# Performance work log

Hardware: AMD Instinct MI355X
Metric: run time of the kernel (lower is better)

The kernel has to match this reference:

```python
import jax, jax.numpy as jnp
import numpy as np


def setup_inputs() -> dict:
    key = jax.random.key(0)
    k1, k2, k3, k4 = jax.random.split(key, 4)
    B, T, C, H = 8, 2048, 768, 64
    x = jax.random.normal(k1, (B, T, C), dtype=jnp.float32)
    # nn.Linear(n_embd, head_size, bias=False): weight [H, C]; stored here as [C, H] for x @ W
    Wk = jax.random.normal(k2, (C, H), dtype=jnp.float32) * (C ** -0.5)
    Wq = jax.random.normal(k3, (C, H), dtype=jnp.float32) * (C ** -0.5)
    Wv = jax.random.normal(k4, (C, H), dtype=jnp.float32) * (C ** -0.5)
    return {"x": x, "Wk": Wk, "Wq": Wq, "Wv": Wv}


def reference(x, Wk, Wq, Wv):
    # x: [B, T, C]
    C = x.shape[-1]
    k = jnp.einsum("btc,ch->bth", x, Wk)  # [B, T, H]
    q = jnp.einsum("btc,ch->bth", x, Wq)  # [B, T, H]
    v = jnp.einsum("btc,ch->bth", x, Wv)  # [B, T, H]
    # NOTE: source scales by C**-0.5 where C = n_embd (input channels), not head_size
    wei = jnp.einsum("bth,bsh->bts", q, k) * (C ** -0.5)  # [B, T, T]
    wei = jax.nn.softmax(wei, axis=-1)
    # dropout p=0.0 (eval): identity
    out = jnp.einsum("bts,bsh->bth", wei, v)  # [B, T, H]
    return out
```

## Files before the change

### kernel.cpp

```cpp
#include <hip/hip_runtime.h>


typedef __attribute__((ext_vector_type(4))) float f32x4;
typedef __attribute__((ext_vector_type(8))) unsigned short u16x8;
typedef __attribute__((ext_vector_type(8))) __bf16 bf16x8;
typedef __attribute__((ext_vector_type(8))) _Float16 f16x8;

#define LDR 72
#define LDT 40
#define KSCALE (0.03608439182435161f * 1.4426950408889634f)
#define PBIAS 4.0f

__device__ __forceinline__ unsigned short f2bf(float f) {
  unsigned int u = __float_as_uint(f);
  u += 0x7FFFu + ((u >> 16) & 1u);
  return (unsigned short)(u >> 16);
}
__device__ __forceinline__ unsigned short hi16(float f) {
  return (unsigned short)(__float_as_uint(f) >> 16);
}
__device__ __forceinline__ f32x4 mfma_bf16(u16x8 a, u16x8 b, f32x4 c) {
  return __builtin_amdgcn_mfma_f32_16x16x32_bf16(
      __builtin_bit_cast(bf16x8, a), __builtin_bit_cast(bf16x8, b), c, 0, 0, 0);
}
__device__ __forceinline__ void cp32B(unsigned short* dst, const unsigned short* src) {
  *(u16x8*)dst = *(const u16x8*)src;
  *(u16x8*)(dst + 8) = *(const u16x8*)(src + 8);
}

__global__ __launch_bounds__(256) void wconv_k(const float* __restrict__ Wk,
                                               const float* __restrict__ Wq,
                                               const float* __restrict__ Wv,
                                               unsigned short* __restrict__ wt) {
  __shared__ unsigned short tr[64 * LDR];
  const int w = blockIdx.x / 12;
  const int kt = blockIdx.x - w * 12;
  const float* W = (w == 0) ? Wk : ((w == 1) ? Wq : Wv);
  const int tid = threadIdx.x;
  const int kr = tid >> 2;
  const int n0 = (tid & 3) * 16;
  const f32x4* src = (const f32x4*)(W + (size_t)(kt * 64 + kr) * 64 + n0);
  f32x4 a0 = src[0], a1 = src[1], a2 = src[2], a3 = src[3];
#pragma unroll
  for (int j = 0; j < 4; ++j) {
    tr[(n0 + j) * LDR + kr] = f2bf(a0[j]);
    tr[(n0 + 4 + j) * LDR + kr] = f2bf(a1[j]);
    tr[(n0 + 8 + j) * LDR + kr] = f2bf(a2[j]);
    tr[(n0 + 12 + j) * LDR + kr] = f2bf(a3[j]);
  }
  __syncthreads();
  const int n = tid >> 2, kc = (tid & 3) * 16;
  cp32B(&wt[(size_t)(w * 64 + n) * 768 + kt * 64 + kc], &tr[n * LDR + kc]);
}

__global__ __launch_bounds__(256) void proj_k(const float* __restrict__ x,
                                              const unsigned short* __restrict__ wt,
                                              unsigned short* __restrict__ kg,
                                              unsigned short* __restrict__ qg,
                                              unsigned short* __restrict__ vt) {
  __shared__ unsigned short x_s[32 * LDR];
  __shared__ unsigned short w_s[192 * LDR];
  __shared__ unsigned short vt_s[64 * LDT];
  const int tid = threadIdx.x;
  const int wv = tid >> 6, lane = tid & 63, c = lane & 15, quad = lane >> 4;
  const int m0 = blockIdx.x * 32;
  const int rowg = wv & 1;
  const int nfb = (wv >> 1) * 6;
  const int srow = tid >> 3;
  const int sc8 = (tid & 7) * 8;

  f32x4 acc[6];
#pragma unroll
  for (int i = 0; i < 6; ++i) acc[i] = f32x4{0.f, 0.f, 0.f, 0.f};

  f32x4 xf0, xf1;
  u16x8 wf[6];
  {
    const f32x4* s = (const f32x4*)(x + (size_t)(m0 + srow) * 768 + sc8);
    xf0 = s[0]; xf1 = s[1];
  }
#pragma unroll
  for (int i = 0; i < 6; ++i)
    wf[i] = *(const u16x8*)&wt[(size_t)(srow + 32 * i) * 768 + sc8];

  for (int kc = 0; kc < 768; kc += 64) {
    {
      u16x8 u;
#pragma unroll
      for (int j = 0; j < 4; ++j) { u[j] = f2bf(xf0[j]); u[4 + j] = f2bf(xf1[j]); }
      *(u16x8*)&x_s[srow * LDR + sc8] = u;
    }
#pragma unroll
    for (int i = 0; i < 6; ++i)
      *(u16x8*)&w_s[(srow + 32 * i) * LDR + sc8] = wf[i];
    __syncthreads();
    if (kc + 64 < 768) {
      const f32x4* s = (const f32x4*)(x + (size_t)(m0 + srow) * 768 + kc + 64 + sc8);
      xf0 = s[0]; xf1 = s[1];
#pragma unroll
      for (int i = 0; i < 6; ++i)
        wf[i] = *(const u16x8*)&wt[(size_t)(srow + 32 * i) * 768 + kc + 64 + sc8];
    }
#pragma unroll
    for (int k32 = 0; k32 < 2; ++k32) {
      u16x8 a = *(const u16x8*)&x_s[(rowg * 16 + c) * LDR + k32 * 32 + quad * 8];
#pragma unroll
      for (int j = 0; j < 6; ++j) {
        u16x8 b = *(const u16x8*)&w_s[((nfb + j) * 16 + c) * LDR + k32 * 32 + quad * 8];
        acc[j] = mfma_bf16(a, b, acc[j]);
      }
    }
    __syncthreads();
  }
  const int r0 = rowg * 16 + quad * 4;
#pragma unroll
  for (int j = 0; j < 6; ++j) {
    const int nf = nfb + j;
    if (nf < 4) {
#pragma unroll
      for (int r = 0; r < 4; ++r)
        kg[(size_t)(m0 + r0 + r) * 64 + nf * 16 + c] = f2bf(acc[j][r]);
    } else if (nf < 8) {
#pragma unroll
      for (int r = 0; r < 4; ++r)
        qg[(size_t)(m0 + r0 + r) * 64 + (nf - 4) * 16 + c] = f2bf(acc[j][r] * KSCALE);
    } else {
#pragma unroll
      for (int r = 0; r < 4; ++r)
        vt_s[((nf - 8) * 16 + c) * LDT + r0 + r] = f2bf(acc[j][r]);
    }
  }
  __syncthreads();
  {
    const int h = tid >> 2, c8 = (tid & 3) * 8;
    const int b = m0 >> 11, tb = m0 & 2047;
    *(u16x8*)(vt + (size_t)b * 131072 + (size_t)h * 2048 + tb + c8) =
        *(const u16x8*)&vt_s[h * LDT + c8];
  }
}

__global__ __launch_bounds__(256, 4) void attn_k(const unsigned short* __restrict__ qg,
                                                 const unsigned short* __restrict__ kg,
                                                 const unsigned short* __restrict__ vt,
                                                 _Float16* __restrict__ part,
                                                 float* __restrict__ lsum) {
  __shared__ unsigned short k_s[64 * LDR];
  __shared__ unsigned short v_s[64 * LDR];
  __shared__ unsigned short p_s[64 * LDR];
  const int tid = threadIdx.x;
  const int wv = tid >> 6, lane = tid & 63, c = lane & 15, quad = lane >> 4;
  const int bq = blockIdx.x;
  const int qt = blockIdx.y;
  const int sc = blockIdx.z;
  const int tq0 = qt * 64;
  const int srow = tid >> 2, sch = (tid & 3) * 16;
  const int s_beg = sc << 9, s_end = s_beg + 512;

  const unsigned short* kbase = kg + (size_t)bq * 131072;
  const unsigned short* vbase = vt + (size_t)bq * 131072;

  u16x8 aq[2];
#pragma unroll
  for (int k32 = 0; k32 < 2; ++k32)
    aq[k32] = *(const u16x8*)(qg + (size_t)(bq * 2048 + tq0 + wv * 16 + c) * 64 +
                              k32 * 32 + quad * 8);

  u16x8 kb0 = *(const u16x8*)(kbase + (size_t)(s_beg + srow) * 64 + sch);
  u16x8 kb1 = *(const u16x8*)(kbase + (size_t)(s_beg + srow) * 64 + sch + 8);
  u16x8 vb0 = *(const u16x8*)(vbase + (size_t)srow * 2048 + s_beg + sch);
  u16x8 vb1 = *(const u16x8*)(vbase + (size_t)srow * 2048 + s_beg + sch + 8);

  u16x8 ones;
#pragma unroll
  for (int j = 0; j < 8; ++j) ones[j] = 0x3F80;

  f32x4 o_acc[4], l_acc;
#pragma unroll
  for (int hf = 0; hf < 4; ++hf) o_acc[hf] = f32x4{0.f, 0.f, 0.f, 0.f};
  l_acc = f32x4{0.f, 0.f, 0.f, 0.f};

  for (int s0 = s_beg; s0 < s_end; s0 += 64) {
    *(u16x8*)&k_s[srow * LDR + sch] = kb0;
    *(u16x8*)&k_s[srow * LDR + sch + 8] = kb1;
    *(u16x8*)&v_s[srow * LDR + sch] = vb0;
    *(u16x8*)&v_s[srow * LDR + sch + 8] = vb1;
    __syncthreads();
    if (s0 + 64 < s_end) {
      kb0 = *(const u16x8*)(kbase + (size_t)(s0 + 64 + srow) * 64 + sch);
      kb1 = *(const u16x8*)(kbase + (size_t)(s0 + 64 + srow) * 64 + sch + 8);
      vb0 = *(const u16x8*)(vbase + (size_t)srow * 2048 + s0 + 64 + sch);
      vb1 = *(const u16x8*)(vbase + (size_t)srow * 2048 + s0 + 64 + sch + 8);
    }
    f32x4 sacc[4];
#pragma unroll
    for (int nf = 0; nf < 4; ++nf) sacc[nf] = f32x4{0.f, 0.f, 0.f, 0.f};
#pragma unroll
    for (int k32 = 0; k32 < 2; ++k32) {
#pragma unroll
      for (int nf = 0; nf < 4; ++nf) {
        u16x8 b = *(const u16x8*)&k_s[(nf * 16 + c) * LDR + k32 * 32 + quad * 8];
        sacc[nf] = mfma_bf16(aq[k32], b, sacc[nf]);
      }
    }
    const int prow = wv * 16 + quad * 4;
#pragma unroll
    for (int nf = 0; nf < 4; ++nf)
#pragma unroll
      for (int r = 0; r < 4; ++r)
        p_s[(prow + r) * LDR + ((nf ^ quad) * 16) + c] =
            hi16(__builtin_amdgcn_exp2f(sacc[nf][r] - PBIAS));
    asm volatile("s_waitcnt lgkmcnt(0)" ::: "memory");
#pragma unroll
    for (int k32 = 0; k32 < 2; ++k32) {
      const int chunkP = (2 * k32 + (quad >> 1)) ^ (c >> 2);
      u16x8 ap = *(const u16x8*)&p_s[(wv * 16 + c) * LDR + chunkP * 16 + (quad & 1) * 8];
#pragma unroll
      for (int hf = 0; hf < 4; ++hf) {
        u16x8 bv = *(const u16x8*)&v_s[(hf * 16 + c) * LDR + k32 * 32 + quad * 8];
        o_acc[hf] = mfma_bf16(ap, bv, o_acc[hf]);
      }
      l_acc = mfma_bf16(ap, ones, l_acc);
    }
    __syncthreads();
  }
  const int pbase = (bq * 32 + qt) * 4 + sc;
  _Float16* po = part + (size_t)pbase * 4096;
#pragma unroll
  for (int hf = 0; hf < 4; ++hf)
#pragma unroll
    for (int r = 0; r < 4; ++r)
      po[(wv * 16 + quad * 4 + r) * 64 + hf * 16 + c] = (_Float16)o_acc[hf][r];
  if (c == 0) {
#pragma unroll
    for (int r = 0; r < 4; ++r)
      lsum[pbase * 64 + wv * 16 + quad * 4 + r] = l_acc[r];
  }
}

__global__ __launch_bounds__(256) void comb_k(const _Float16* __restrict__ part,
                                              const float* __restrict__ lsum,
                                              float* __restrict__ out) {
  const int bq = blockIdx.x, qh = blockIdx.y;
  const int qt = qh >> 1;
  const int row = (qh & 1) * 32 + (threadIdx.x >> 3);
  const int h0 = (threadIdx.x & 7) * 8;
  const int base = (bq * 32 + qt) * 4;
  float acc[8];
#pragma unroll
  for (int j = 0; j < 8; ++j) acc[j] = 0.f;
  float l = 0.f;
#pragma unroll
  for (int c4 = 0; c4 < 4; ++c4) {
    l += lsum[(base + c4) * 64 + row];
    f16x8 p = *(const f16x8*)(part + (size_t)(base + c4) * 4096 + row * 64 + h0);
#pragma unroll
    for (int j = 0; j < 8; ++j) acc[j] += (float)p[j];
  }
  const float inv = 1.0f / l;
  float* op = out + (size_t)(bq * 2048 + qt * 64 + row) * 64 + h0;
#pragma unroll
  for (int j = 0; j < 8; ++j) op[j] = acc[j] * inv;
}

extern "C" void kernel_launch(void* const* d_in, const int* in_sizes, int n_in,
                              void* d_out, int out_size, void* d_ws, size_t ws_size,
                              hipStream_t stream) {
  const float* x = (const float*)d_in[0];
  const float* Wk = (const float*)d_in[1];
  const float* Wq = (const float*)d_in[2];
  const float* Wv = (const float*)d_in[3];
  char* ws = (char*)d_ws;
  unsigned short* kg = (unsigned short*)(ws);
  unsigned short* qg = (unsigned short*)(ws + (size_t)(2 << 20));
  unsigned short* vt = (unsigned short*)(ws + (size_t)(4 << 20));
  unsigned short* wt = (unsigned short*)(ws + (size_t)(6 << 20));
  _Float16* part = (_Float16*)(ws + (size_t)(7 << 20));
  float* lsum = (float*)(ws + (size_t)(15 << 20));
  float* out = (float*)d_out;

  hipLaunchKernelGGL(wconv_k, dim3(36), dim3(256), 0, stream, Wk, Wq, Wv, wt);
  hipLaunchKernelGGL(proj_k, dim3(512), dim3(256), 0, stream, x, wt, kg, qg, vt);
  hipLaunchKernelGGL(attn_k, dim3(8, 32, 4), dim3(256), 0, stream, qg, kg, vt, part, lsum);
  hipLaunchKernelGGL(comb_k, dim3(8, 64), dim3(256), 0, stream, part, lsum, out);
}
```

Measured before the change: 121.6 us.

## Fuse split-KV combine into attention kernel via last-block atomic counter

Drops the separate combine kernel. Each attention block now increments a per-query-tile atomic counter after writing its partial output, and the last of the four split blocks reduces the partials and writes the normalized result. The wconv kernel gets an extra block that zeroes the counters. This saves one kernel launch and its tail, at the cost of threadfences, an atomic per block, and a serialized combine tail inside the attention grid.

```diff
diff --git a/kernel.cpp b/kernel.cpp
--- a/kernel.cpp
+++ b/kernel.cpp
@@ -31,12 +31,14 @@
 __global__ __launch_bounds__(256) void wconv_k(const float* __restrict__ Wk,
                                                const float* __restrict__ Wq,
                                                const float* __restrict__ Wv,
-                                               unsigned short* __restrict__ wt) {
+                                               unsigned short* __restrict__ wt,
+                                               int* __restrict__ cnt) {
   __shared__ unsigned short tr[64 * LDR];
+  const int tid = threadIdx.x;
+  if (blockIdx.x == 36) { cnt[tid] = 0; return; }
   const int w = blockIdx.x / 12;
   const int kt = blockIdx.x - w * 12;
   const float* W = (w == 0) ? Wk : ((w == 1) ? Wq : Wv);
-  const int tid = threadIdx.x;
   const int kr = tid >> 2;
   const int n0 = (tid & 3) * 16;
   const f32x4* src = (const f32x4*)(W + (size_t)(kt * 64 + kr) * 64 + n0);
@@ -143,10 +145,13 @@
                                                  const unsigned short* __restrict__ kg,
                                                  const unsigned short* __restrict__ vt,
                                                  _Float16* __restrict__ part,
-                                                 float* __restrict__ lsum) {
+                                                 float* __restrict__ lsum,
+                                                 int* __restrict__ cnt,
+                                                 float* __restrict__ out) {
   __shared__ unsigned short k_s[64 * LDR];
   __shared__ unsigned short v_s[64 * LDR];
   __shared__ unsigned short p_s[64 * LDR];
+  __shared__ int done_flag;
   const int tid = threadIdx.x;
   const int wv = tid >> 6, lane = tid & 63, c = lane & 15, quad = lane >> 4;
   const int bq = blockIdx.x;
@@ -223,7 +228,8 @@
     }
     __syncthreads();
   }
-  const int pbase = (bq * 32 + qt) * 4 + sc;
+  const int cidx = bq * 32 + qt;
+  const int pbase = cidx * 4 + sc;
   _Float16* po = part + (size_t)pbase * 4096;
 #pragma unroll
   for (int hf = 0; hf < 4; ++hf)
@@ -235,31 +241,39 @@
     for (int r = 0; r < 4; ++r)
       lsum[pbase * 64 + wv * 16 + quad * 4 + r] = l_acc[r];
   }
-}
-
-__global__ __launch_bounds__(256) void comb_k(const _Float16* __restrict__ part,
-                                              const float* __restrict__ lsum,
-                                              float* __restrict__ out) {
-  const int bq = blockIdx.x, qh = blockIdx.y;
-  const int qt = qh >> 1;
-  const int row = (qh & 1) * 32 + (threadIdx.x >> 3);
-  const int h0 = (threadIdx.x & 7) * 8;
-  const int base = (bq * 32 + qt) * 4;
-  float acc[8];
-#pragma unroll
-  for (int j = 0; j < 8; ++j) acc[j] = 0.f;
-  float l = 0.f;
-#pragma unroll
-  for (int c4 = 0; c4 < 4; ++c4) {
-    l += lsum[(base + c4) * 64 + row];
-    f16x8 p = *(const f16x8*)(part + (size_t)(base + c4) * 4096 + row * 64 + h0);
-#pragma unroll
-    for (int j = 0; j < 8; ++j) acc[j] += (float)p[j];
-  }
-  const float inv = 1.0f / l;
-  float* op = out + (size_t)(bq * 2048 + qt * 64 + row) * 64 + h0;
-#pragma unroll
-  for (int j = 0; j < 8; ++j) op[j] = acc[j] * inv;
+  __threadfence();
+  __syncthreads();
+  if (tid == 0)
+    done_flag = (__hip_atomic_fetch_add(&cnt[cidx], 1, __ATOMIC_ACQ_REL,
+                                        __HIP_MEMORY_SCOPE_AGENT) == 3);
+  __syncthreads();
+  if (done_flag) {
+    __threadfence();
+    const int row = tid >> 2, h0 = (tid & 3) * 16;
+    float a[16];
+#pragma unroll
+    for (int j = 0; j < 16; ++j) a[j] = 0.f;
+    float l = 0.f;
+#pragma unroll
+    for (int c4 = 0; c4 < 4; ++c4) {
+      const int pb = cidx * 4 + c4;
+      l += lsum[pb * 64 + row];
+      const _Float16* pp = part + (size_t)pb * 4096 + row * 64 + h0;
+      f16x8 p0 = *(const f16x8*)pp;
+      f16x8 p1 = *(const f16x8*)(pp + 8);
+#pragma unroll
+      for (int j = 0; j < 8; ++j) { a[j] += (float)p0[j]; a[8 + j] += (float)p1[j]; }
+    }
+    const float inv = 1.0f / l;
+    float* op = out + (size_t)(bq * 2048 + tq0 + row) * 64 + h0;
+#pragma unroll
+    for (int v4 = 0; v4 < 4; ++v4) {
+      f32x4 o;
+#pragma unroll
+      for (int j = 0; j < 4; ++j) o[j] = a[v4 * 4 + j] * inv;
+      *(f32x4*)(op + v4 * 4) = o;
+    }
+  }
 }
 
 extern "C" void kernel_launch(void* const* d_in, const int* in_sizes, int n_in,
@@ -276,10 +290,11 @@
   unsigned short* wt = (unsigned short*)(ws + (size_t)(6 << 20));
   _Float16* part = (_Float16*)(ws + (size_t)(7 << 20));
   float* lsum = (float*)(ws + (size_t)(15 << 20));
+  int* cnt = (int*)(ws + (size_t)(15 << 20) + (size_t)(256 << 10));
   float* out = (float*)d_out;
 
-  hipLaunchKernelGGL(wconv_k, dim3(36), dim3(256), 0, stream, Wk, Wq, Wv, wt);
+  hipLaunchKernelGGL(wconv_k, dim3(37), dim3(256), 0, stream, Wk, Wq, Wv, wt, cnt);
   hipLaunchKernelGGL(proj_k, dim3(512), dim3(256), 0, stream, x, wt, kg, qg, vt);
-  hipLaunchKernelGGL(attn_k, dim3(8, 32, 4), dim3(256), 0, stream, qg, kg, vt, part, lsum);
-  hipLaunchKernelGGL(comb_k, dim3(8, 64), dim3(256), 0, stream, part, lsum, out);
-}
+  hipLaunchKernelGGL(attn_k, dim3(8, 32, 4), dim3(256), 0, stream, qg, kg, vt, part,
+                     lsum, cnt, out);
+}
```

New measurement: 268.8 us. +121.1%, slower.
